# Performance work log

Measured on AMD Instinct MI355X. Metric: run time of the kernel, lower is better.

The kernel has to match this reference:

```python
import jax, jax.numpy as jnp
from jax import lax
import numpy as np

B, TQ, T = 64, 2, 2048
HID, ENC, U, FILT, K = 1024, 512, 256, 32, 31


def setup_inputs() -> dict:
    key = jax.random.key(0)
    ks = jax.random.split(key, 12)
    def w(k, shape, fan_in):
        return jax.random.normal(k, shape, jnp.float32) / np.sqrt(fan_in)
    return {
        "query": jax.random.normal(ks[0], (B, TQ, HID), jnp.float32),
        "state": jax.random.uniform(ks[1], (B, T), jnp.float32),
        "memory": jax.random.normal(ks[2], (B, T, ENC), jnp.float32),
        "Wq": w(ks[3], (HID, U), HID), "bq": jnp.zeros((U,), jnp.float32),
        "Wm": w(ks[4], (ENC, U), ENC), "bm": jnp.zeros((U,), jnp.float32),
        "Wl": w(ks[5], (FILT, U), FILT), "bl": jnp.zeros((U,), jnp.float32),
        "conv_w": w(ks[6], (FILT, 1, K), K), "conv_b": jnp.zeros((FILT,), jnp.float32),
        "We": w(ks[7], (U, U), U), "be": jnp.zeros((U,), jnp.float32),
        "v_a": w(ks[8], (U,), U),
    }


def reference(query, state, memory, Wq, bq, Wm, bm, Wl, bl, conv_w, conv_b, We, be, v_a):
    # memory projection (done in `initialize` in the original): [B,T,U]
    mem_proj = jnp.einsum("bte,eu->btu", memory, Wm) + bm
    # query projection then slice timestep 1 -> [B,1,U]
    pq = (jnp.einsum("bqh,hu->bqu", query, Wq) + bq)[:, 1:2, :]
    # location features: 1-D conv over time of previous alignment, 'same' padding
    x = state[:, None, :]                                    # [B,1,T]
    f = lax.conv_general_dilated(x, conv_w, (1,), "SAME",
                                 dimension_numbers=("NCH", "OIH", "NCH"))
    f = f + conv_b[None, :, None]                            # [B,FILT,T]
    loc = jnp.einsum("bft,fu->btu", f, Wl) + bl              # [B,T,U]
    # additive energy with tanh, reduced against v_a -> [B,T]
    h = jnp.tanh(jnp.einsum("btu,uv->btv", pq + loc + mem_proj, We) + be)
    energy = jnp.einsum("btu,u->bt", h, v_a)
    # smoothing normalization: sigmoid / sum(sigmoid)
    s = jax.nn.sigmoid(energy)
    alignment = s / jnp.sum(s, axis=-1, keepdims=True)
    # cumulate_weights=True: accumulate onto previous alignment
    cum_alignment = state + alignment
    # context against projected memory: [B,1,U]
    context = jnp.einsum("bt,btu->bu", cum_alignment, mem_proj)[:, None, :]
    return context
```

## Files before the change

kernel.cpp:

```cpp
#include <hip/hip_runtime.h>
#include <hip/hip_bf16.h>
#include <math.h>

#define Bq 64
#define Tt 2048
#define TQn 2
#define HIDn 1024
#define ENCn 512
#define Un 256
#define FILTn 32
#define KKn 31

#define TTILE 32
#define NCHUNK (Tt / TTILE)

typedef short short8 __attribute__((ext_vector_type(8)));
typedef float f32x4  __attribute__((ext_vector_type(4)));
typedef unsigned short ushort_t;
typedef unsigned int   uint_t;

union S8 { short8 v; uint_t u[4]; };

__device__ __forceinline__ ushort_t f2b(float f) {
    union { float f; uint_t u; } x; x.f = f;
    uint_t r = x.u + 0x7fffu + ((x.u >> 16) & 1u);
    return (ushort_t)(r >> 16);
}
__device__ __forceinline__ uint_t cvt_pk(float lo, float hi) {
    union { __hip_bfloat162 h; uint_t u; } x;
    x.h = __float22bfloat162_rn(make_float2(lo, hi));
    return x.u;
}
__device__ __forceinline__ float tanh_fast(float x) {
    const float e = __expf(2.0f * x);
    return 1.0f - 2.0f * __builtin_amdgcn_rcpf(e + 1.0f);
}

__device__ __forceinline__ int bp_idx(int v, int k) {
    const int seg = (k >> 5) * 16 + (v >> 6) * 4 + ((v >> 4) & 3);
    const int ln  = ((k >> 3) & 3) * 16 + (v & 15);
    return seg * 512 + ln * 8 + (k & 7);
}

__global__ void k_prep1(const float* __restrict__ We, const float* __restrict__ Wm,
                        const float* __restrict__ Wl, const float* __restrict__ conv_w,
                        const float* __restrict__ bq, const float* __restrict__ bm,
                        const float* __restrict__ bl, const float* __restrict__ conv_b,
                        ushort_t* __restrict__ Bp, ushort_t* __restrict__ CWT,
                        float* __restrict__ cvec)
{
    const int blk = blockIdx.x;
    const int v = threadIdx.x;
    if (blk < 512) {
        const int e = blk;
        float a0 = 0.f, a1 = 0.f, a2 = 0.f, a3 = 0.f;
        #pragma unroll 4
        for (int u = 0; u < Un; u += 4) {
            a0 += Wm[(size_t)e * Un + u + 0] * We[(u + 0) * Un + v];
            a1 += Wm[(size_t)e * Un + u + 1] * We[(u + 1) * Un + v];
            a2 += Wm[(size_t)e * Un + u + 2] * We[(u + 2) * Un + v];
            a3 += Wm[(size_t)e * Un + u + 3] * We[(u + 3) * Un + v];
        }
        Bp[bp_idx(v, e)] = f2b((a0 + a1) + (a2 + a3));
    } else if (blk < 516) {
        const int vc = (blk - 512) * 64;
        __shared__ float wlwe[FILTn * 64];
        for (int i = threadIdx.x; i < FILTn * 64; i += 256) {
            const int f = i >> 6, vv = i & 63;
            float a = 0.f;
            #pragma unroll 8
            for (int u = 0; u < Un; ++u) a += Wl[f * Un + u] * We[u * Un + vc + vv];
            wlwe[f * 64 + vv] = a;
        }
        __syncthreads();
        for (int i = threadIdx.x; i < 64 * 32; i += 256) {
            const int vv = i >> 5, k = i & 31;
            float a = 0.f;
            if (k < KKn) {
                #pragma unroll
                for (int f = 0; f < FILTn; ++f) a += conv_w[f * KKn + k] * wlwe[f * 64 + vv];
            }
            CWT[bp_idx(vc + vv, k)] = f2b(a);
        }
    } else {
        const int u = v;
        float a = bq[u] + bm[u] + bl[u];
        #pragma unroll
        for (int f = 0; f < FILTn; ++f) a += conv_b[f] * Wl[f * Un + u];
        cvec[u] = a;
    }
}

__global__ void k_g(const float* __restrict__ query, const float* __restrict__ Wq,
                    const float* __restrict__ cvec, float* __restrict__ g)
{
    const int b = blockIdx.x, hs = blockIdx.y * 128, u = threadIdx.x;
    const float* q = query + ((size_t)b * TQn + 1) * HIDn + hs;
    float a0 = 0.f, a1 = 0.f, a2 = 0.f, a3 = 0.f;
    #pragma unroll 4
    for (int h = 0; h < 128; h += 4) {
        a0 += q[h + 0] * Wq[(size_t)(hs + h + 0) * Un + u];
        a1 += q[h + 1] * Wq[(size_t)(hs + h + 1) * Un + u];
        a2 += q[h + 2] * Wq[(size_t)(hs + h + 2) * Un + u];
        a3 += q[h + 3] * Wq[(size_t)(hs + h + 3) * Un + u];
    }
    float acc = (a0 + a1) + (a2 + a3);
    if (blockIdx.y == 0) acc += cvec[u];
    atomicAdd(&g[b * Un + u], acc);
}

__global__ void k_zconst(const float* __restrict__ g, const float* __restrict__ We,
                         const float* __restrict__ be, float* __restrict__ zconst)
{
    const int b = blockIdx.x, us = blockIdx.y * 64, v = threadIdx.x;
    float a0 = 0.f, a1 = 0.f;
    #pragma unroll 4
    for (int u = us; u < us + 64; u += 2) {
        a0 += g[b * Un + u]     * We[(size_t)u * Un + v];
        a1 += g[b * Un + u + 1] * We[(size_t)(u + 1) * Un + v];
    }
    float acc = a0 + a1;
    if (blockIdx.y == 0) acc += be[v];
    atomicAdd(&zconst[b * Un + v], acc);
}

__global__ __launch_bounds__(256, 4) void attn_main(
    const float* __restrict__ memory, const float* __restrict__ state,
    const ushort_t* __restrict__ Bp, const ushort_t* __restrict__ CWT,
    const float* __restrict__ zconst, const float* __restrict__ v_a,
    float* __restrict__ zA, float* __restrict__ zS,
    float* __restrict__ zSsum, float* __restrict__ zStsum)
{
    const int blk = blockIdx.x;
    const int b  = blk >> 6;
    const int c  = blk & (NCHUNK - 1);
    const int t0 = c * TTILE;
    const int tid = threadIdx.x;

    __shared__ __align__(16) float sw_raw[80];
    __shared__ __align__(16) float ep_s[4][TTILE];
    __shared__ __align__(16) float s_s[TTILE];
    float* sw = sw_raw + 1;

    for (int i = tid; i < TTILE + 31; i += 256) {
        const int t = t0 - 15 + i;
        sw[i] = (t >= 0 && t < Tt) ? state[b * Tt + t] : 0.0f;
    }

    const int lane = tid & 63;
    const int w    = tid >> 6;
    const int lm   = lane & 15;
    const int lq   = lane >> 4;
    const int ncol0 = w * 64 + lm;

    const ushort_t* bp0 = Bp + (size_t)(w * 4) * 512 + lane * 8;
    const ushort_t* bp1 = bp0 + 512;
    const ushort_t* bp2 = bp0 + 1024;
    const ushort_t* bp3 = bp0 + 1536;
    const ushort_t* cp0 = CWT + (size_t)(w * 4) * 512 + lane * 8;

    short8 bbuf[2][4];
    bbuf[0][0] = *(const short8*)(bp0);
    bbuf[0][1] = *(const short8*)(bp1);
    bbuf[0][2] = *(const short8*)(bp2);
    bbuf[0][3] = *(const short8*)(bp3);
    bbuf[1][0] = *(const short8*)(bp0 + 8192);
    bbuf[1][1] = *(const short8*)(bp1 + 8192);
    bbuf[1][2] = *(const short8*)(bp2 + 8192);
    bbuf[1][3] = *(const short8*)(bp3 + 8192);

    const float* gA0 = memory + ((size_t)b * Tt + t0 + lm) * ENCn + lq * 8;
    const float* gA1 = gA0 + 16 * ENCn;

    float4 n00 = *(const float4*)(gA0);
    float4 n01 = *(const float4*)(gA0 + 4);
    float4 n10 = *(const float4*)(gA1);
    float4 n11 = *(const float4*)(gA1 + 4);

    f32x4 acc[2][4] = {};

    __syncthreads();

    S8 a0c, a1c;
    a0c.u[0] = cvt_pk(n00.x, n00.y); a0c.u[1] = cvt_pk(n00.z, n00.w);
    a0c.u[2] = cvt_pk(n01.x, n01.y); a0c.u[3] = cvt_pk(n01.z, n01.w);
    a1c.u[0] = cvt_pk(n10.x, n10.y); a1c.u[1] = cvt_pk(n10.z, n10.w);
    a1c.u[2] = cvt_pk(n11.x, n11.y); a1c.u[3] = cvt_pk(n11.z, n11.w);

    #pragma unroll
    for (int s = 0; s < 16; ++s) {
        const int sa = ((s + 1) & 15) * 32;
        n00 = *(const float4*)(gA0 + sa);
        n01 = *(const float4*)(gA0 + sa + 4);
        n10 = *(const float4*)(gA1 + sa);
        n11 = *(const float4*)(gA1 + sa + 4);
        acc[0][0] = __builtin_amdgcn_mfma_f32_16x16x32_bf16(a0c.v, bbuf[s & 1][0], acc[0][0], 0, 0, 0);
        acc[0][1] = __builtin_amdgcn_mfma_f32_16x16x32_bf16(a0c.v, bbuf[s & 1][1], acc[0][1], 0, 0, 0);
        acc[0][2] = __builtin_amdgcn_mfma_f32_16x16x32_bf16(a0c.v, bbuf[s & 1][2], acc[0][2], 0, 0, 0);
        acc[0][3] = __builtin_amdgcn_mfma_f32_16x16x32_bf16(a0c.v, bbuf[s & 1][3], acc[0][3], 0, 0, 0);
        acc[1][0] = __builtin_amdgcn_mfma_f32_16x16x32_bf16(a1c.v, bbuf[s & 1][0], acc[1][0], 0, 0, 0);
        acc[1][1] = __builtin_amdgcn_mfma_f32_16x16x32_bf16(a1c.v, bbuf[s & 1][1], acc[1][1], 0, 0, 0);
        acc[1][2] = __builtin_amdgcn_mfma_f32_16x16x32_bf16(a1c.v, bbuf[s & 1][2], acc[1][2], 0, 0, 0);
        acc[1][3] = __builtin_amdgcn_mfma_f32_16x16x32_bf16(a1c.v, bbuf[s & 1][3], acc[1][3], 0, 0, 0);
        const int sn = ((s + 2) & 15) * 8192;
        bbuf[s & 1][0] = *(const short8*)(bp0 + sn);
        bbuf[s & 1][1] = *(const short8*)(bp1 + sn);
        bbuf[s & 1][2] = *(const short8*)(bp2 + sn);
        bbuf[s & 1][3] = *(const short8*)(bp3 + sn);
        a0c.u[0] = cvt_pk(n00.x, n00.y); a0c.u[1] = cvt_pk(n00.z, n00.w);
        a0c.u[2] = cvt_pk(n01.x, n01.y); a0c.u[3] = cvt_pk(n01.z, n01.w);
        a1c.u[0] = cvt_pk(n10.x, n10.y); a1c.u[1] = cvt_pk(n10.z, n10.w);
        a1c.u[2] = cvt_pk(n11.x, n11.y); a1c.u[3] = cvt_pk(n11.z, n11.w);
    }

    {
        S8 ca0, ca1;
        #pragma unroll
        for (int j = 0; j < 4; ++j) {
            const int base0 = lm + lq * 8 + 2 * j;
            ca0.u[j] = cvt_pk(sw[base0],      sw[base0 + 1]);
            ca1.u[j] = cvt_pk(sw[base0 + 16], sw[base0 + 17]);
        }
        const short8 cb0 = *(const short8*)(cp0);
        const short8 cb1 = *(const short8*)(cp0 + 512);
        const short8 cb2 = *(const short8*)(cp0 + 1024);
        const short8 cb3 = *(const short8*)(cp0 + 1536);
        acc[0][0] = __builtin_amdgcn_mfma_f32_16x16x32_bf16(ca0.v, cb0, acc[0][0], 0, 0, 0);
        acc[0][1] = __builtin_amdgcn_mfma_f32_16x16x32_bf16(ca0.v, cb1, acc[0][1], 0, 0, 0);
        acc[0][2] = __builtin_amdgcn_mfma_f32_16x16x32_bf16(ca0.v, cb2, acc[0][2], 0, 0, 0);
        acc[0][3] = __builtin_amdgcn_mfma_f32_16x16x32_bf16(ca0.v, cb3, acc[0][3], 0, 0, 0);
        acc[1][0] = __builtin_amdgcn_mfma_f32_16x16x32_bf16(ca1.v, cb0, acc[1][0], 0, 0, 0);
        acc[1][1] = __builtin_amdgcn_mfma_f32_16x16x32_bf16(ca1.v, cb1, acc[1][1], 0, 0, 0);
        acc[1][2] = __builtin_amdgcn_mfma_f32_16x16x32_bf16(ca1.v, cb2, acc[1][2], 0, 0, 0);
        acc[1][3] = __builtin_amdgcn_mfma_f32_16x16x32_bf16(ca1.v, cb3, acc[1][3], 0, 0, 0);
    }

    float zc[4], va[4];
    #pragma unroll
    for (int nbi = 0; nbi < 4; ++nbi) {
        const int col = ncol0 + nbi * 16;
        zc[nbi] = zconst[b * Un + col];
        va[nbi] = v_a[col];
    }
    #pragma unroll
    for (int mb = 0; mb < 2; ++mb) {
        #pragma unroll
        for (int r = 0; r < 4; ++r) {
            float ep = 0.f;
            #pragma unroll
            for (int nbi = 0; nbi < 4; ++nbi)
                ep += tanh_fast(acc[mb][nbi][r] + zc[nbi]) * va[nbi];
            ep += __shfl_xor(ep, 1, 64);
            ep += __shfl_xor(ep, 2, 64);
            ep += __shfl_xor(ep, 4, 64);
            ep += __shfl_xor(ep, 8, 64);
            if (lm == 0) ep_s[w][mb * 16 + lq * 4 + r] = ep;
        }
    }
    __syncthreads();

    if (tid < 64) {
        float s = 0.f, st = 0.f;
        if (tid < TTILE) {
            const float energy = ep_s[0][tid] + ep_s[1][tid] + ep_s[2][tid] + ep_s[3][tid];
            s = __builtin_amdgcn_rcpf(1.0f + __expf(-energy));
            s_s[tid] = s;
            st = sw[15 + tid];
        }
        float ssum = s, stsum = st;
        #pragma unroll
        for (int off = 32; off >= 1; off >>= 1) {
            ssum  += __shfl_xor(ssum,  off, 64);
            stsum += __shfl_xor(stsum, off, 64);
        }
        if (tid == 0) {
            atomicAdd(&zSsum[b], ssum);
            atomicAdd(&zStsum[b], stsum);
        }
    }
    __syncthreads();

    const int e0 = tid << 1;
    const float* gM = memory + ((size_t)b * Tt + t0) * ENCn + e0;
    float aA0 = 0.f, aA1 = 0.f, aS0 = 0.f, aS1 = 0.f;
    #pragma unroll 4
    for (int r = 0; r < TTILE; ++r) {
        const float2 mm = *(const float2*)(gM + (size_t)r * ENCn);
        const float st = sw[15 + r];
        const float sv = s_s[r];
        aA0 += st * mm.x; aA1 += st * mm.y;
        aS0 += sv * mm.x; aS1 += sv * mm.y;
    }
    atomicAdd(&zA[b * ENCn + e0],     aA0);
    atomicAdd(&zA[b * ENCn + e0 + 1], aA1);
    atomicAdd(&zS[b * ENCn + e0],     aS0);
    atomicAdd(&zS[b * ENCn + e0 + 1], aS1);
}

__global__ void k_final(const float* __restrict__ zA, const float* __restrict__ zS,
                        const float* __restrict__ zSsum, const float* __restrict__ zStsum,
                        const float* __restrict__ Wm, const float* __restrict__ bm,
                        float* __restrict__ out)
{
    const int b = blockIdx.x, e0 = blockIdx.y * 128, u = threadIdx.x;
    const float inv = 1.0f / zSsum[b];
    float a0 = 0.f, a1 = 0.f;
    #pragma unroll 4
    for (int e = e0; e < e0 + 128; e += 2) {
        const float c0 = zA[b * ENCn + e]     + zS[b * ENCn + e]     * inv;
        const float c1 = zA[b * ENCn + e + 1] + zS[b * ENCn + e + 1] * inv;
        a0 += c0 * Wm[(size_t)e * Un + u];
        a1 += c1 * Wm[(size_t)(e + 1) * Un + u];
    }
    float acc = a0 + a1;
    if (blockIdx.y == 0) acc += bm[u] * (zStsum[b] + 1.0f);
    atomicAdd(&out[b * Un + u], acc);
}

extern "C" void kernel_launch(void* const* d_in, const int* in_sizes, int n_in,
                              void* d_out, int out_size, void* d_ws, size_t ws_size,
                              hipStream_t stream)
{
    const float* query  = (const float*)d_in[0];
    const float* state  = (const float*)d_in[1];
    const float* memory = (const float*)d_in[2];
    const float* Wq     = (const float*)d_in[3];
    const float* bq     = (const float*)d_in[4];
    const float* Wm     = (const float*)d_in[5];
    const float* bm     = (const float*)d_in[6];
    const float* Wl     = (const float*)d_in[7];
    const float* bl     = (const float*)d_in[8];
    const float* conv_w = (const float*)d_in[9];
    const float* conv_b = (const float*)d_in[10];
    const float* We     = (const float*)d_in[11];
    const float* be     = (const float*)d_in[12];
    const float* v_a    = (const float*)d_in[13];
    float* out = (float*)d_out;

    float* ws      = (float*)d_ws;
    float* zA      = ws;
    float* zS      = ws + 32768;
    float* zSsum   = ws + 65536;
    float* zStsum  = ws + 65600;
    float* g_      = ws + 65664;
    float* zconst  = ws + 82048;
    float* cvec    = ws + 98432;
    ushort_t* Bp    = (ushort_t*)(ws + 98688);
    ushort_t* CWT   = (ushort_t*)(ws + 164224);

    hipMemsetAsync(ws, 0, 98432 * sizeof(float), stream);
    hipMemsetAsync(out, 0, (size_t)Bq * Un * sizeof(float), stream);

    hipLaunchKernelGGL(k_prep1, dim3(517), dim3(Un), 0, stream,
                       We, Wm, Wl, conv_w, bq, bm, bl, conv_b, Bp, CWT, cvec);
    hipLaunchKernelGGL(k_g, dim3(Bq, 8), dim3(Un), 0, stream, query, Wq, cvec, g_);
    hipLaunchKernelGGL(k_zconst, dim3(Bq, 4), dim3(Un), 0, stream, g_, We, be, zconst);
    hipLaunchKernelGGL(attn_main, dim3(Bq * NCHUNK), dim3(256), 0, stream,
                       memory, state, Bp, CWT, zconst, v_a, zA, zS, zSsum, zStsum);
    hipLaunchKernelGGL(k_final, dim3(Bq, 4), dim3(Un), 0, stream,
                       zA, zS, zSsum, zStsum, Wm, bm, out);
}
```

Before: 608.4 us.

## Fuse query and zconst prep into one kernel; double attention time tile

Merges the cvec, query-projection and zconst kernels into a single prep kernel that has 64 extra blocks, each computing one batch's projected query vector in LDS. This removes two launches and the atomics on g. The main attention kernel now handles 64 timesteps per block instead of 32. Each B-fragment load is reused across four M-tiles, launch bounds drop to 3 blocks per SM, and the context loop reads s and state as float4. The cost is higher register pressure, fewer blocks in flight, and a serial 1024-long dot product inside each per-batch prep block.

New measurement: 577.5 us. 5.1% less time.

```diff
diff --git a/kernel.cpp b/kernel.cpp
--- a/kernel.cpp
+++ b/kernel.cpp
@@ -11,7 +11,7 @@
 #define FILTn 32
 #define KKn 31
 
-#define TTILE 32
+#define TTILE 64
 #define NCHUNK (Tt / TTILE)
 
 typedef short short8 __attribute__((ext_vector_type(8)));
@@ -42,16 +42,20 @@
     return seg * 512 + ln * 8 + (k & 7);
 }
 
-__global__ void k_prep1(const float* __restrict__ We, const float* __restrict__ Wm,
-                        const float* __restrict__ Wl, const float* __restrict__ conv_w,
-                        const float* __restrict__ bq, const float* __restrict__ bm,
-                        const float* __restrict__ bl, const float* __restrict__ conv_b,
-                        ushort_t* __restrict__ Bp, ushort_t* __restrict__ CWT,
-                        float* __restrict__ cvec)
+__global__ void k_prep(const float* __restrict__ We, const float* __restrict__ Wm,
+                       const float* __restrict__ Wl, const float* __restrict__ conv_w,
+                       const float* __restrict__ bq, const float* __restrict__ bm,
+                       const float* __restrict__ bl, const float* __restrict__ conv_b,
+                       const float* __restrict__ query, const float* __restrict__ Wq,
+                       const float* __restrict__ be,
+                       ushort_t* __restrict__ Bp, ushort_t* __restrict__ CWT,
+                       float* __restrict__ zconst)
 {
     const int blk = blockIdx.x;
-    const int v = threadIdx.x;
+    __shared__ float wlwe[FILTn * 64];
+    __shared__ float g_lds[Un];
     if (blk < 512) {
+        const int v = threadIdx.x;
         const int e = blk;
         float a0 = 0.f, a1 = 0.f, a2 = 0.f, a3 = 0.f;
         #pragma unroll 4
@@ -64,7 +68,6 @@
         Bp[bp_idx(v, e)] = f2b((a0 + a1) + (a2 + a3));
     } else if (blk < 516) {
         const int vc = (blk - 512) * 64;
-        __shared__ float wlwe[FILTn * 64];
         for (int i = threadIdx.x; i < FILTn * 64; i += 256) {
             const int f = i >> 6, vv = i & 63;
             float a = 0.f;
@@ -83,48 +86,33 @@
             CWT[bp_idx(vc + vv, k)] = f2b(a);
         }
     } else {
-        const int u = v;
-        float a = bq[u] + bm[u] + bl[u];
-        #pragma unroll
-        for (int f = 0; f < FILTn; ++f) a += conv_b[f] * Wl[f * Un + u];
-        cvec[u] = a;
-    }
-}
-
-__global__ void k_g(const float* __restrict__ query, const float* __restrict__ Wq,
-                    const float* __restrict__ cvec, float* __restrict__ g)
-{
-    const int b = blockIdx.x, hs = blockIdx.y * 128, u = threadIdx.x;
-    const float* q = query + ((size_t)b * TQn + 1) * HIDn + hs;
-    float a0 = 0.f, a1 = 0.f, a2 = 0.f, a3 = 0.f;
-    #pragma unroll 4
-    for (int h = 0; h < 128; h += 4) {
-        a0 += q[h + 0] * Wq[(size_t)(hs + h + 0) * Un + u];
-        a1 += q[h + 1] * Wq[(size_t)(hs + h + 1) * Un + u];
-        a2 += q[h + 2] * Wq[(size_t)(hs + h + 2) * Un + u];
-        a3 += q[h + 3] * Wq[(size_t)(hs + h + 3) * Un + u];
-    }
-    float acc = (a0 + a1) + (a2 + a3);
-    if (blockIdx.y == 0) acc += cvec[u];
-    atomicAdd(&g[b * Un + u], acc);
-}
-
-__global__ void k_zconst(const float* __restrict__ g, const float* __restrict__ We,
-                         const float* __restrict__ be, float* __restrict__ zconst)
-{
-    const int b = blockIdx.x, us = blockIdx.y * 64, v = threadIdx.x;
-    float a0 = 0.f, a1 = 0.f;
-    #pragma unroll 4
-    for (int u = us; u < us + 64; u += 2) {
-        a0 += g[b * Un + u]     * We[(size_t)u * Un + v];
-        a1 += g[b * Un + u + 1] * We[(size_t)(u + 1) * Un + v];
-    }
-    float acc = a0 + a1;
-    if (blockIdx.y == 0) acc += be[v];
-    atomicAdd(&zconst[b * Un + v], acc);
-}
-
-__global__ __launch_bounds__(256, 4) void attn_main(
+        const int b = blk - 516;
+        const int u = threadIdx.x;
+        float cv = bq[u] + bm[u] + bl[u];
+        #pragma unroll
+        for (int f = 0; f < FILTn; ++f) cv += conv_b[f] * Wl[f * Un + u];
+        const float* q = query + ((size_t)b * TQn + 1) * HIDn;
+        float a0 = 0.f, a1 = 0.f, a2 = 0.f, a3 = 0.f;
+        #pragma unroll 4
+        for (int h = 0; h < HIDn; h += 4) {
+            a0 += q[h + 0] * Wq[(size_t)(h + 0) * Un + u];
+            a1 += q[h + 1] * Wq[(size_t)(h + 1) * Un + u];
+            a2 += q[h + 2] * Wq[(size_t)(h + 2) * Un + u];
+            a3 += q[h + 3] * Wq[(size_t)(h + 3) * Un + u];
+        }
+        g_lds[u] = cv + (a0 + a1) + (a2 + a3);
+        __syncthreads();
+        float z0 = 0.f, z1 = 0.f;
+        #pragma unroll 4
+        for (int uu = 0; uu < Un; uu += 2) {
+            z0 += g_lds[uu]     * We[(size_t)uu * Un + u];
+            z1 += g_lds[uu + 1] * We[(size_t)(uu + 1) * Un + u];
+        }
+        zconst[b * Un + u] = be[u] + z0 + z1;
+    }
+}
+
+__global__ __launch_bounds__(256, 3) void attn_main(
     const float* __restrict__ memory, const float* __restrict__ state,
     const ushort_t* __restrict__ Bp, const ushort_t* __restrict__ CWT,
     const float* __restrict__ zconst, const float* __restrict__ v_a,
@@ -132,12 +120,12 @@
     float* __restrict__ zSsum, float* __restrict__ zStsum)
 {
     const int blk = blockIdx.x;
-    const int b  = blk >> 6;
+    const int b  = blk >> 5;
     const int c  = blk & (NCHUNK - 1);
     const int t0 = c * TTILE;
     const int tid = threadIdx.x;
 
-    __shared__ __align__(16) float sw_raw[80];
+    __shared__ __align__(16) float sw_raw[TTILE + 36];
     __shared__ __align__(16) float ep_s[4][TTILE];
     __shared__ __align__(16) float s_s[TTILE];
     float* sw = sw_raw + 1;
@@ -169,70 +157,77 @@
     bbuf[1][2] = *(const short8*)(bp2 + 8192);
     bbuf[1][3] = *(const short8*)(bp3 + 8192);
 
-    const float* gA0 = memory + ((size_t)b * Tt + t0 + lm) * ENCn + lq * 8;
-    const float* gA1 = gA0 + 16 * ENCn;
-
-    float4 n00 = *(const float4*)(gA0);
-    float4 n01 = *(const float4*)(gA0 + 4);
-    float4 n10 = *(const float4*)(gA1);
-    float4 n11 = *(const float4*)(gA1 + 4);
-
-    f32x4 acc[2][4] = {};
+    const float* gAb = memory + ((size_t)b * Tt + t0 + lm) * ENCn + lq * 8;
+
+    float4 nx[4][2];
+    #pragma unroll
+    for (int i = 0; i < 4; ++i) {
+        nx[i][0] = *(const float4*)(gAb + (size_t)i * 16 * ENCn);
+        nx[i][1] = *(const float4*)(gAb + (size_t)i * 16 * ENCn + 4);
+    }
+
+    f32x4 acc[4][4] = {};
 
     __syncthreads();
 
-    S8 a0c, a1c;
-    a0c.u[0] = cvt_pk(n00.x, n00.y); a0c.u[1] = cvt_pk(n00.z, n00.w);
-    a0c.u[2] = cvt_pk(n01.x, n01.y); a0c.u[3] = cvt_pk(n01.z, n01.w);
-    a1c.u[0] = cvt_pk(n10.x, n10.y); a1c.u[1] = cvt_pk(n10.z, n10.w);
-    a1c.u[2] = cvt_pk(n11.x, n11.y); a1c.u[3] = cvt_pk(n11.z, n11.w);
+    S8 af[4];
+    #pragma unroll
+    for (int i = 0; i < 4; ++i) {
+        af[i].u[0] = cvt_pk(nx[i][0].x, nx[i][0].y);
+        af[i].u[1] = cvt_pk(nx[i][0].z, nx[i][0].w);
+        af[i].u[2] = cvt_pk(nx[i][1].x, nx[i][1].y);
+        af[i].u[3] = cvt_pk(nx[i][1].z, nx[i][1].w);
+    }
 
     #pragma unroll
     for (int s = 0; s < 16; ++s) {
         const int sa = ((s + 1) & 15) * 32;
-        n00 = *(const float4*)(gA0 + sa);
-        n01 = *(const float4*)(gA0 + sa + 4);
-        n10 = *(const float4*)(gA1 + sa);
-        n11 = *(const float4*)(gA1 + sa + 4);
-        acc[0][0] = __builtin_amdgcn_mfma_f32_16x16x32_bf16(a0c.v, bbuf[s & 1][0], acc[0][0], 0, 0, 0);
-        acc[0][1] = __builtin_amdgcn_mfma_f32_16x16x32_bf16(a0c.v, bbuf[s & 1][1], acc[0][1], 0, 0, 0);
-        acc[0][2] = __builtin_amdgcn_mfma_f32_16x16x32_bf16(a0c.v, bbuf[s & 1][2], acc[0][2], 0, 0, 0);
-        acc[0][3] = __builtin_amdgcn_mfma_f32_16x16x32_bf16(a0c.v, bbuf[s & 1][3], acc[0][3], 0, 0, 0);
-        acc[1][0] = __builtin_amdgcn_mfma_f32_16x16x32_bf16(a1c.v, bbuf[s & 1][0], acc[1][0], 0, 0, 0);
-        acc[1][1] = __builtin_amdgcn_mfma_f32_16x16x32_bf16(a1c.v, bbuf[s & 1][1], acc[1][1], 0, 0, 0);
-        acc[1][2] = __builtin_amdgcn_mfma_f32_16x16x32_bf16(a1c.v, bbuf[s & 1][2], acc[1][2], 0, 0, 0);
-        acc[1][3] = __builtin_amdgcn_mfma_f32_16x16x32_bf16(a1c.v, bbuf[s & 1][3], acc[1][3], 0, 0, 0);
+        #pragma unroll
+        for (int i = 0; i < 4; ++i) {
+            nx[i][0] = *(const float4*)(gAb + (size_t)i * 16 * ENCn + sa);
+            nx[i][1] = *(const float4*)(gAb + (size_t)i * 16 * ENCn + sa + 4);
+        }
+        #pragma unroll
+        for (int i = 0; i < 4; ++i) {
+            #pragma unroll
+            for (int n = 0; n < 4; ++n)
+                acc[i][n] = __builtin_amdgcn_mfma_f32_16x16x32_bf16(af[i].v, bbuf[s & 1][n], acc[i][n], 0, 0, 0);
+        }
         const int sn = ((s + 2) & 15) * 8192;
         bbuf[s & 1][0] = *(const short8*)(bp0 + sn);
         bbuf[s & 1][1] = *(const short8*)(bp1 + sn);
         bbuf[s & 1][2] = *(const short8*)(bp2 + sn);
         bbuf[s & 1][3] = *(const short8*)(bp3 + sn);
-        a0c.u[0] = cvt_pk(n00.x, n00.y); a0c.u[1] = cvt_pk(n00.z, n00.w);
-        a0c.u[2] = cvt_pk(n01.x, n01.y); a0c.u[3] = cvt_pk(n01.z, n01.w);
-        a1c.u[0] = cvt_pk(n10.x, n10.y); a1c.u[1] = cvt_pk(n10.z, n10.w);
-        a1c.u[2] = cvt_pk(n11.x, n11.y); a1c.u[3] = cvt_pk(n11.z, n11.w);
+        #pragma unroll
+        for (int i = 0; i < 4; ++i) {
+            af[i].u[0] = cvt_pk(nx[i][0].x, nx[i][0].y);
+            af[i].u[1] = cvt_pk(nx[i][0].z, nx[i][0].w);
+            af[i].u[2] = cvt_pk(nx[i][1].x, nx[i][1].y);
+            af[i].u[3] = cvt_pk(nx[i][1].z, nx[i][1].w);
+        }
     }
 
     {
-        S8 ca0, ca1;
-        #pragma unroll
-        for (int j = 0; j < 4; ++j) {
-            const int base0 = lm + lq * 8 + 2 * j;
-            ca0.u[j] = cvt_pk(sw[base0],      sw[base0 + 1]);
-            ca1.u[j] = cvt_pk(sw[base0 + 16], sw[base0 + 17]);
+        S8 ca[4];
+        #pragma unroll
+        for (int i = 0; i < 4; ++i) {
+            #pragma unroll
+            for (int j = 0; j < 4; ++j) {
+                const int base0 = lm + 16 * i + lq * 8 + 2 * j;
+                ca[i].u[j] = cvt_pk(sw[base0], sw[base0 + 1]);
+            }
         }
         const short8 cb0 = *(const short8*)(cp0);
         const short8 cb1 = *(const short8*)(cp0 + 512);
         const short8 cb2 = *(const short8*)(cp0 + 1024);
         const short8 cb3 = *(const short8*)(cp0 + 1536);
-        acc[0][0] = __builtin_amdgcn_mfma_f32_16x16x32_bf16(ca0.v, cb0, acc[0][0], 0, 0, 0);
-        acc[0][1] = __builtin_amdgcn_mfma_f32_16x16x32_bf16(ca0.v, cb1, acc[0][1], 0, 0, 0);
-        acc[0][2] = __builtin_amdgcn_mfma_f32_16x16x32_bf16(ca0.v, cb2, acc[0][2], 0, 0, 0);
-        acc[0][3] = __builtin_amdgcn_mfma_f32_16x16x32_bf16(ca0.v, cb3, acc[0][3], 0, 0, 0);
-        acc[1][0] = __builtin_amdgcn_mfma_f32_16x16x32_bf16(ca1.v, cb0, acc[1][0], 0, 0, 0);
-        acc[1][1] = __builtin_amdgcn_mfma_f32_16x16x32_bf16(ca1.v, cb1, acc[1][1], 0, 0, 0);
-        acc[1][2] = __builtin_amdgcn_mfma_f32_16x16x32_bf16(ca1.v, cb2, acc[1][2], 0, 0, 0);
-        acc[1][3] = __builtin_amdgcn_mfma_f32_16x16x32_bf16(ca1.v, cb3, acc[1][3], 0, 0, 0);
+        #pragma unroll
+        for (int i = 0; i < 4; ++i) {
+            acc[i][0] = __builtin_amdgcn_mfma_f32_16x16x32_bf16(ca[i].v, cb0, acc[i][0], 0, 0, 0);
+            acc[i][1] = __builtin_amdgcn_mfma_f32_16x16x32_bf16(ca[i].v, cb1, acc[i][1], 0, 0, 0);
+            acc[i][2] = __builtin_amdgcn_mfma_f32_16x16x32_bf16(ca[i].v, cb2, acc[i][2], 0, 0, 0);
+            acc[i][3] = __builtin_amdgcn_mfma_f32_16x16x32_bf16(ca[i].v, cb3, acc[i][3], 0, 0, 0);
+        }
     }
 
     float zc[4], va[4];
@@ -243,30 +238,27 @@
         va[nbi] = v_a[col];
     }
     #pragma unroll
-    for (int mb = 0; mb < 2; ++mb) {
+    for (int i = 0; i < 4; ++i) {
         #pragma unroll
         for (int r = 0; r < 4; ++r) {
             float ep = 0.f;
             #pragma unroll
             for (int nbi = 0; nbi < 4; ++nbi)
-                ep += tanh_fast(acc[mb][nbi][r] + zc[nbi]) * va[nbi];
+                ep += tanh_fast(acc[i][nbi][r] + zc[nbi]) * va[nbi];
             ep += __shfl_xor(ep, 1, 64);
             ep += __shfl_xor(ep, 2, 64);
             ep += __shfl_xor(ep, 4, 64);
             ep += __shfl_xor(ep, 8, 64);
-            if (lm == 0) ep_s[w][mb * 16 + lq * 4 + r] = ep;
+            if (lm == 0) ep_s[w][i * 16 + lq * 4 + r] = ep;
         }
     }
     __syncthreads();
 
     if (tid < 64) {
-        float s = 0.f, st = 0.f;
-        if (tid < TTILE) {
-            const float energy = ep_s[0][tid] + ep_s[1][tid] + ep_s[2][tid] + ep_s[3][tid];
-            s = __builtin_amdgcn_rcpf(1.0f + __expf(-energy));
-            s_s[tid] = s;
-            st = sw[15 + tid];
-        }
+        const float energy = ep_s[0][tid] + ep_s[1][tid] + ep_s[2][tid] + ep_s[3][tid];
+        const float s = __builtin_amdgcn_rcpf(1.0f + __expf(-energy));
+        s_s[tid] = s;
+        const float st = sw[15 + tid];
         float ssum = s, stsum = st;
         #pragma unroll
         for (int off = 32; off >= 1; off >>= 1) {
@@ -283,13 +275,19 @@
     const int e0 = tid << 1;
     const float* gM = memory + ((size_t)b * Tt + t0) * ENCn + e0;
     float aA0 = 0.f, aA1 = 0.f, aS0 = 0.f, aS1 = 0.f;
-    #pragma unroll 4
-    for (int r = 0; r < TTILE; ++r) {
-        const float2 mm = *(const float2*)(gM + (size_t)r * ENCn);
-        const float st = sw[15 + r];
-        const float sv = s_s[r];
-        aA0 += st * mm.x; aA1 += st * mm.y;
-        aS0 += sv * mm.x; aS1 += sv * mm.y;
+    #pragma unroll 2
+    for (int r4 = 0; r4 < TTILE / 4; ++r4) {
+        const float4 sv4 = *(const float4*)&s_s[r4 * 4];
+        const float4 st4 = *(const float4*)&sw[15 + r4 * 4];
+        const float sv[4] = {sv4.x, sv4.y, sv4.z, sv4.w};
+        const float st[4] = {st4.x, st4.y, st4.z, st4.w};
+        #pragma unroll
+        for (int j = 0; j < 4; ++j) {
+            const int r = r4 * 4 + j;
+            const float2 mm = *(const float2*)(gM + (size_t)r * ENCn);
+            aA0 += st[j] * mm.x; aA1 += st[j] * mm.y;
+            aS0 += sv[j] * mm.x; aS1 += sv[j] * mm.y;
+        }
     }
     atomicAdd(&zA[b * ENCn + e0],     aA0);
     atomicAdd(&zA[b * ENCn + e0 + 1], aA1);
@@ -342,19 +340,16 @@
     float* zS      = ws + 32768;
     float* zSsum   = ws + 65536;
     float* zStsum  = ws + 65600;
-    float* g_      = ws + 65664;
-    float* zconst  = ws + 82048;
-    float* cvec    = ws + 98432;
-    ushort_t* Bp    = (ushort_t*)(ws + 98688);
-    ushort_t* CWT   = (ushort_t*)(ws + 164224);
-
-    hipMemsetAsync(ws, 0, 98432 * sizeof(float), stream);
+    float* zconst  = ws + 65664;
+    ushort_t* Bp    = (ushort_t*)(ws + 82048);
+    ushort_t* CWT   = (ushort_t*)(ws + 147584);
+
+    hipMemsetAsync(ws, 0, 65664 * sizeof(float), stream);
     hipMemsetAsync(out, 0, (size_t)Bq * Un * sizeof(float), stream);
 
-    hipLaunchKernelGGL(k_prep1, dim3(517), dim3(Un), 0, stream,
-                       We, Wm, Wl, conv_w, bq, bm, bl, conv_b, Bp, CWT, cvec);
-    hipLaunchKernelGGL(k_g, dim3(Bq, 8), dim3(Un), 0, stream, query, Wq, cvec, g_);
-    hipLaunchKernelGGL(k_zconst, dim3(Bq, 4), dim3(Un), 0, stream, g_, We, be, zconst);
+    hipLaunchKernelGGL(k_prep, dim3(516 + Bq), dim3(Un), 0, stream,
+                       We, Wm, Wl, conv_w, bq, bm, bl, conv_b, query, Wq, be,
+                       Bp, CWT, zconst);
     hipLaunchKernelGGL(attn_main, dim3(Bq * NCHUNK), dim3(256), 0, stream,
                        memory, state, Bp, CWT, zconst, v_a, zA, zS, zSsum, zStsum);
     hipLaunchKernelGGL(k_final, dim3(Bq, 4), dim3(Un), 0, stream,
```
